# Performance work log

Measured on AMD Instinct MI355X. Metric: run time of the kernel, lower is better.

## Reference

```python
import jax, jax.numpy as jnp
import numpy as np

B, S, E, H = 2, 2048, 1024, 16
HD = E // H

def setup_inputs() -> dict:
    key = jax.random.key(0)
    ks = jax.random.split(key, 12)
    q = jax.random.normal(ks[0], (B, S, E), jnp.float32)
    k = jax.random.normal(ks[1], (B, S, E), jnp.float32)
    v = jax.random.normal(ks[2], (B, S, E), jnp.float32)
    # causal mask: 1.0 where attention is disallowed (upper triangle)
    mask = jnp.triu(jnp.ones((S, S), jnp.float32), k=1)[None, None, :, :]
    w = lambda kk: jax.random.normal(kk, (E, E), jnp.float32) * 0.02
    return {
        "q": q, "k": k, "v": v, "mask": mask,
        "Wq": w(ks[3]), "bq": jnp.zeros((E,), jnp.float32),
        "Wk": w(ks[4]), "bk": jnp.zeros((E,), jnp.float32),
        "Wv": w(ks[5]), "bv": jnp.zeros((E,), jnp.float32),
        "Wz": w(ks[6]), "bz": jnp.zeros((E,), jnp.float32),
    }

def _create_heads(x):
    # Faithful to tf.reshape(tf.transpose(x), (B, H, -1, HD)):
    # tf.transpose reverses all dims: [B,S,E] -> [E,S,B], then reshape.
    return jnp.transpose(x, (2, 1, 0)).reshape(B, H, -1, HD)

def reference(q, k, v, mask, Wq, bq, Wk, bk, Wv, bv, Wz, bz):
    qh = _create_heads(q @ Wq + bq)  # (B,H,S,HD)
    kh = _create_heads(k @ Wk + bk)
    vh = _create_heads(v @ Wv + bv)
    qn = qh / jnp.linalg.norm(qh, axis=-1, keepdims=True)
    kn = kh / jnp.linalg.norm(kh, axis=-1, keepdims=True)
    logits = jnp.einsum('bhqd,bhkd->bhqk', qn, kn) * 1000.0
    logits = logits + mask * -1000000000.0
    attn = jax.nn.softmax(logits, axis=-1)  # (B,H,S,S)
    z = jnp.einsum('bhqk,bhkd->bhqd', attn, vh)
    zc = jnp.transpose(z, (0, 2, 1, 3)).reshape(B, -1, E)
    return zc @ Wz + bz, attn
```

## Files before the change

### kernel.cpp

```cpp
#include <hip/hip_runtime.h>
#include <cstdint>
#include <cstddef>


typedef __bf16 bf16x4 __attribute__((ext_vector_type(4)));
typedef __bf16 bf16x8 __attribute__((ext_vector_type(8)));
typedef float floatx4 __attribute__((ext_vector_type(4)));

#define GLOAD_LDS16(g, l)                                                      \
    __builtin_amdgcn_global_load_lds(                                          \
        (const __attribute__((address_space(1))) void*)(g),                    \
        (__attribute__((address_space(3))) void*)(l), 16, 0, 0)

__global__ __launch_bounds__(256) void split_a(
    const float* __restrict__ x0, const float* __restrict__ x1,
    const float* __restrict__ x2, __bf16* __restrict__ ApBase)
{
    const float* X = blockIdx.z == 0 ? x0 : (blockIdx.z == 1 ? x1 : x2);
    __bf16* Ap = ApBase + (size_t)blockIdx.z * (4096ull * 2048);
    const int idx = blockIdx.x * 256 + threadIdx.x;
    const int r = idx >> 8;
    const int c = (idx & 255) * 4;
    float4 t = *(const float4*)(X + (size_t)r * 1024 + c);
    bf16x4 hi, lo;
    hi[0] = (__bf16)t.x; lo[0] = (__bf16)(t.x - (float)hi[0]);
    hi[1] = (__bf16)t.y; lo[1] = (__bf16)(t.y - (float)hi[1]);
    hi[2] = (__bf16)t.z; lo[2] = (__bf16)(t.z - (float)hi[2]);
    hi[3] = (__bf16)t.w; lo[3] = (__bf16)(t.w - (float)hi[3]);
    *(bf16x4*)(Ap + (size_t)r * 2048 + c) = hi;
    *(bf16x4*)(Ap + (size_t)r * 2048 + 1024 + c) = lo;
}

__global__ __launch_bounds__(256) void split_bt(
    const float* __restrict__ w0, const float* __restrict__ w1,
    const float* __restrict__ w2, __bf16* __restrict__ dstBase, size_t dstStride)
{
    const float* W = blockIdx.z == 0 ? w0 : (blockIdx.z == 1 ? w1 : w2);
    __bf16* Bp = dstBase + (size_t)blockIdx.z * dstStride;
    __shared__ float tile[64][65];
    const int tid = (int)threadIdx.x;
    const int k0 = blockIdx.y * 64, n0 = blockIdx.x * 64;
    #pragma unroll
    for (int p = 0; p < 4; ++p) {
        int kr = p * 16 + (tid >> 4);
        float4 t = *(const float4*)(W + (size_t)(k0 + kr) * 1024 + n0 + (tid & 15) * 4);
        tile[kr][(tid & 15) * 4 + 0] = t.x; tile[kr][(tid & 15) * 4 + 1] = t.y;
        tile[kr][(tid & 15) * 4 + 2] = t.z; tile[kr][(tid & 15) * 4 + 3] = t.w;
    }
    __syncthreads();
    const int nr = tid >> 2, kc = (tid & 3) * 16;
    bf16x8 hi0, hi1, lo0, lo1;
    #pragma unroll
    for (int j = 0; j < 8; ++j) {
        float x = tile[kc + j][nr];
        __bf16 h = (__bf16)x; hi0[j] = h; lo0[j] = (__bf16)(x - (float)h);
        float y = tile[kc + 8 + j][nr];
        __bf16 g = (__bf16)y; hi1[j] = g; lo1[j] = (__bf16)(y - (float)g);
    }
    __bf16* row = Bp + (size_t)(n0 + nr) * 2048;
    *(bf16x8*)(row + k0 + kc)          = hi0;
    *(bf16x8*)(row + k0 + kc + 8)      = hi1;
    *(bf16x8*)(row + 1024 + k0 + kc)     = lo0;
    *(bf16x8*)(row + 1024 + k0 + kc + 8) = lo1;
}

__global__ __launch_bounds__(256) void gemm_split(
    const __bf16* __restrict__ Ap0, const __bf16* __restrict__ Bp0,
    const float* __restrict__ b0, const float* __restrict__ b1,
    const float* __restrict__ b2, float* __restrict__ Out0,
    int transposeOut)
{
    const int z = blockIdx.z;
    const __bf16* Ap = Ap0 + (size_t)z * (4096ull * 2048);
    const __bf16* Bp = Bp0 + (size_t)z * (1024ull * 2048);
    const float* bias = z == 0 ? b0 : (z == 1 ? b1 : b2);
    float* Out = Out0 + (size_t)z * (4096ull * 1024);

    __shared__ __bf16 As[2 * 128 * 32];
    __shared__ __bf16 Bs[2 * 128 * 32];

    const int tid = (int)threadIdx.x;
    const int wave = tid >> 6, lane = tid & 63;
    const int quad = lane >> 4, tl = lane & 15;
    const int m0 = blockIdx.y * 128, n0 = blockIdx.x * 128;
    const int waveM = wave >> 1, waveN = wave & 1;

    floatx4 acc[4][4];
    #pragma unroll
    for (int i = 0; i < 4; ++i)
        #pragma unroll
        for (int j = 0; j < 4; ++j)
            acc[i][j] = (floatx4){0.f, 0.f, 0.f, 0.f};

    const int sRow  = (wave << 4) + (lane >> 2);
    const int sColB = (lane & 3) << 4;
    auto* AsL = (__attribute__((address_space(3))) char*)As;
    auto* BsL = (__attribute__((address_space(3))) char*)Bs;
    const int ldsOff = wave * 1024;

    for (int k0 = 0; k0 < 1024; k0 += 32) {
        __syncthreads();
        #pragma unroll
        for (int i = 0; i < 2; ++i) {
            GLOAD_LDS16((const char*)(Ap + (size_t)(m0 + i*64 + sRow) * 2048 + k0) + sColB,
                        AsL + i * 4096 + ldsOff);
            GLOAD_LDS16((const char*)(Ap + 1024 + (size_t)(m0 + i*64 + sRow) * 2048 + k0) + sColB,
                        AsL + 8192 + i * 4096 + ldsOff);
            GLOAD_LDS16((const char*)(Bp + (size_t)(n0 + i*64 + sRow) * 2048 + k0) + sColB,
                        BsL + i * 4096 + ldsOff);
            GLOAD_LDS16((const char*)(Bp + 1024 + (size_t)(n0 + i*64 + sRow) * 2048 + k0) + sColB,
                        BsL + 8192 + i * 4096 + ldsOff);
        }
        __syncthreads();

        bf16x8 ah[4], bh[4], al[4], bl[4];
        #pragma unroll
        for (int mt = 0; mt < 4; ++mt)
            ah[mt] = *(const bf16x8*)(As + (waveM*64 + mt*16 + tl) * 32 + quad * 8);
        #pragma unroll
        for (int nt = 0; nt < 4; ++nt)
            bh[nt] = *(const bf16x8*)(Bs + (waveN*64 + nt*16 + tl) * 32 + quad * 8);
        #pragma unroll
        for (int mt = 0; mt < 4; ++mt)
            #pragma unroll
            for (int nt = 0; nt < 4; ++nt)
                acc[mt][nt] = __builtin_amdgcn_mfma_f32_16x16x32_bf16(
                    ah[mt], bh[nt], acc[mt][nt], 0, 0, 0);
        #pragma unroll
        for (int mt = 0; mt < 4; ++mt)
            al[mt] = *(const bf16x8*)(As + 4096 + (waveM*64 + mt*16 + tl) * 32 + quad * 8);
        #pragma unroll
        for (int mt = 0; mt < 4; ++mt)
            #pragma unroll
            for (int nt = 0; nt < 4; ++nt)
                acc[mt][nt] = __builtin_amdgcn_mfma_f32_16x16x32_bf16(
                    al[mt], bh[nt], acc[mt][nt], 0, 0, 0);
        #pragma unroll
        for (int nt = 0; nt < 4; ++nt)
            bl[nt] = *(const bf16x8*)(Bs + 4096 + (waveN*64 + nt*16 + tl) * 32 + quad * 8);
        #pragma unroll
        for (int mt = 0; mt < 4; ++mt)
            #pragma unroll
            for (int nt = 0; nt < 4; ++nt)
                acc[mt][nt] = __builtin_amdgcn_mfma_f32_16x16x32_bf16(
                    ah[mt], bl[nt], acc[mt][nt], 0, 0, 0);
    }

    if (transposeOut) {
        #pragma unroll
        for (int nt = 0; nt < 4; ++nt) {
            const int e = n0 + waveN * 64 + nt * 16 + tl;
            const float bb = bias[e];
            #pragma unroll
            for (int mt = 0; mt < 4; ++mt) {
                floatx4 v = acc[mt][nt] + bb;
                *(floatx4*)(Out + (size_t)e * 4096 + m0 + waveM * 64 + mt * 16 + quad * 4) = v;
            }
        }
    } else {
        #pragma unroll
        for (int mt = 0; mt < 4; ++mt) {
            const int rbase = m0 + waveM * 64 + mt * 16 + quad * 4;
            #pragma unroll
            for (int nt = 0; nt < 4; ++nt) {
                const int e = n0 + waveN * 64 + nt * 16 + tl;
                const float bb = bias[e];
                #pragma unroll
                for (int reg = 0; reg < 4; ++reg)
                    Out[(size_t)(rbase + reg) * 1024 + e] = acc[mt][nt][reg] + bb;
            }
        }
    }
}

__global__ __launch_bounds__(256) void gather_qk(
    const float* __restrict__ PT, __bf16* __restrict__ Outp)
{
    const int tid  = (int)threadIdx.x;
    const int lane = tid & 63;
    const int vec  = blockIdx.x * 4 + (tid >> 6);
    const int head = vec >> 11;
    const int sp   = vec & 2047;
    const int c    = (head >> 4) * 512 + (head & 15) * 32 + (sp >> 6);
    const int src  = (lane & 1) * 2048 + (sp & 63) * 32 + (lane >> 1);
    float v = PT[(size_t)c * 4096 + src];
    float ss = v * v;
    #pragma unroll
    for (int mk = 32; mk >= 1; mk >>= 1) ss += __shfl_xor(ss, mk);
    v = v / sqrtf(ss);
    __bf16 h = (__bf16)v;
    Outp[(size_t)vec * 128 + lane]      = h;
    Outp[(size_t)vec * 128 + 64 + lane] = (__bf16)(v - (float)h);
}

__global__ __launch_bounds__(256) void v_transpose(
    const float* __restrict__ PTv, __bf16* __restrict__ Vt)
{
    const int head = blockIdx.y, st = blockIdx.x;
    const int tid = (int)threadIdx.x;
    const int c = (head >> 4) * 512 + (head & 15) * 32 + st;
    const float* __restrict__ row = PTv + (size_t)c * 4096;

    __shared__ float tile[64][65];
    #pragma unroll
    for (int i = 0; i < 4; ++i) {
        int o = i * 1024 + tid * 4;
        float4 t = *(const float4*)(row + o);
        float vals[4] = {t.x, t.y, t.z, t.w};
        #pragma unroll
        for (int e = 0; e < 4; ++e) {
            int oo = o + e;
            int d  = ((oo & 2047) & 31) * 2 + (oo >> 11);
            int sl = (oo & 2047) >> 5;
            tile[sl][d] = vals[e];
        }
    }
    __syncthreads();

    const int d = tid >> 2, jb = (tid & 3) * 16;
    bf16x8 h0, h1, l0, l1;
    #pragma unroll
    for (int j = 0; j < 8; ++j) {
        float x = tile[jb + j][d];
        __bf16 hh = (__bf16)x; h0[j] = hh; l0[j] = (__bf16)(x - (float)hh);
        float y = tile[jb + 8 + j][d];
        __bf16 gg = (__bf16)y; h1[j] = gg; l1[j] = (__bf16)(y - (float)gg);
    }
    size_t bh = ((size_t)head * 128 + d) * 2048 + st * 64 + jb;
    size_t bl = ((size_t)head * 128 + 64 + d) * 2048 + st * 64 + jb;
    *(bf16x8*)(Vt + bh)     = h0;
    *(bf16x8*)(Vt + bh + 8) = h1;
    *(bf16x8*)(Vt + bl)     = l0;
    *(bf16x8*)(Vt + bl + 8) = l1;
}

__global__ __launch_bounds__(512, 4) void attn_mfma(
    const __bf16* __restrict__ Qp, const __bf16* __restrict__ Kp,
    const __bf16* __restrict__ Vt, float* __restrict__ Attn,
    __bf16* __restrict__ Az)
{
    const int flat = (int)blockIdx.x;
    const int head = flat & 31;
    const int it   = 15 - (flat >> 5);
    const int tid = (int)threadIdx.x;
    const int w = tid >> 6, lane = tid & 63;
    const int quad = lane >> 4, tl = lane & 15;
    const int t7 = tl & 7;
    const int i0 = it * 128;
    const int jtmax = 2 * it + 1;
    const int wrowMax = i0 + w * 16 + 15;
    const int wdiag   = (i0 + w * 16) >> 6;

    const __bf16* __restrict__ Qh = Qp + ((size_t)head * 2048 + i0) * 128;
    const __bf16* __restrict__ Kh = Kp + (size_t)head * 2048 * 128;
    const __bf16* __restrict__ Vh = Vt + (size_t)head * 128 * 2048;
    float* __restrict__ Ah = Attn + (size_t)head * ((size_t)2048 * 2048);

    __shared__ __bf16 kb[64 * 128];
    __shared__ __bf16 vt[128 * 64];
    __shared__ __bf16 ps[8][16 * 72];
    __bf16* psw = ps[w];
    auto* kbL = (__attribute__((address_space(3))) char*)kb;
    auto* vtL = (__attribute__((address_space(3))) char*)vt;

    const char* kSrc[2];
    const char* vSrc[2];
    #pragma unroll
    for (int i = 0; i < 2; ++i) {
        int d  = i * 512 + tid;
        int rK = d >> 4, cK = (d & 15) ^ (rK & 7);
        kSrc[i] = (const char*)(Kh + (size_t)rK * 128) + cK * 16;
        int rV = d >> 3, cV = (d & 7) ^ (rV & 7);
        vSrc[i] = (const char*)(Vh + (size_t)rV * 2048) + cV * 16;
    }
    const int ok0 = ((quad)      ^ t7) * 8;
    const int ok1 = ((quad + 4)  ^ t7) * 8;
    const int ok2 = ((quad + 8)  ^ t7) * 8;
    const int ok3 = ((quad + 12) ^ t7) * 8;

    const __bf16* qrow = Qh + (size_t)(w * 16 + tl) * 128;
    bf16x8 qhi0 = *(const bf16x8*)(qrow + quad * 8);
    bf16x8 qhi1 = *(const bf16x8*)(qrow + 32 + quad * 8);
    bf16x8 qlo0 = *(const bf16x8*)(qrow + 64 + quad * 8);
    bf16x8 qlo1 = *(const bf16x8*)(qrow + 96 + quad * 8);

    for (int jt = jtmax + 1; jt < 32; ++jt) {
        float4 z4 = make_float4(0.f, 0.f, 0.f, 0.f);
        #pragma unroll
        for (int g = 0; g < 4; ++g)
            *(float4*)(Ah + (size_t)(i0 + w * 16 + g * 4 + quad) * 2048
                          + jt * 64 + tl * 4) = z4;
    }

    float m[4], l[4];
    #pragma unroll
    for (int r = 0; r < 4; ++r) { m[r] = -3.0e38f; l[r] = 0.0f; }

    for (int jt = 0; jt <= jtmax; ++jt) {
        __syncthreads();
        #pragma unroll
        for (int i = 0; i < 2; ++i)
            GLOAD_LDS16(kSrc[i] + (size_t)jt * 16384, kbL + i * 8192 + w * 1024);
        __syncthreads();
        if (jt * 64 > wrowMax) continue;

        floatx4 S[4];
        #pragma unroll
        for (int sub = 0; sub < 4; ++sub) {
            const __bf16* kr = kb + (sub * 16 + tl) * 128;
            bf16x8 khi0 = *(const bf16x8*)(kr + ok0);
            bf16x8 khi1 = *(const bf16x8*)(kr + ok1);
            bf16x8 klo0 = *(const bf16x8*)(kr + ok2);
            bf16x8 klo1 = *(const bf16x8*)(kr + ok3);
            floatx4 s = (floatx4){0.f, 0.f, 0.f, 0.f};
            s = __builtin_amdgcn_mfma_f32_16x16x32_bf16(qhi0, khi0, s, 0, 0, 0);
            s = __builtin_amdgcn_mfma_f32_16x16x32_bf16(qhi1, khi1, s, 0, 0, 0);
            s = __builtin_amdgcn_mfma_f32_16x16x32_bf16(qhi0, klo0, s, 0, 0, 0);
            s = __builtin_amdgcn_mfma_f32_16x16x32_bf16(qhi1, klo1, s, 0, 0, 0);
            s = __builtin_amdgcn_mfma_f32_16x16x32_bf16(qlo0, khi0, s, 0, 0, 0);
            s = __builtin_amdgcn_mfma_f32_16x16x32_bf16(qlo1, khi1, s, 0, 0, 0);
            S[sub] = s;
        }
        const bool diag = (jt == wdiag);
        #pragma unroll
        for (int reg = 0; reg < 4; ++reg) {
            const int irow = w * 16 + quad * 4 + reg;
            float sl[4];
            #pragma unroll
            for (int sub = 0; sub < 4; ++sub) {
                float lv = S[sub][reg] * 1000.0f;
                if (diag && (jt * 64 + sub * 16 + tl > i0 + irow)) lv = -1.0e9f;
                sl[sub] = lv;
            }
            float mt = fmaxf(fmaxf(sl[0], sl[1]), fmaxf(sl[2], sl[3]));
            float mn = fmaxf(m[reg], mt);
            l[reg] = l[reg] * __expf(m[reg] - mn)
                   + __expf(sl[0]-mn) + __expf(sl[1]-mn)
                   + __expf(sl[2]-mn) + __expf(sl[3]-mn);
            m[reg] = mn;
        }
    }

    #pragma unroll
    for (int reg = 0; reg < 4; ++reg) {
        #pragma unroll
        for (int mk = 8; mk >= 1; mk >>= 1) {
            float mo = __shfl_xor(m[reg], mk);
            float lo = __shfl_xor(l[reg], mk);
            float mn = fmaxf(m[reg], mo);
            l[reg] = l[reg] * __expf(m[reg] - mn) + lo * __expf(mo - mn);
            m[reg] = mn;
        }
    }
    float inv_l[4];
    #pragma unroll
    for (int reg = 0; reg < 4; ++reg) inv_l[reg] = 1.0f / l[reg];

    floatx4 zacc[4];
    #pragma unroll
    for (int t = 0; t < 4; ++t) zacc[t] = (floatx4){0.f, 0.f, 0.f, 0.f};

    for (int jt = 0; jt <= jtmax; ++jt) {
        __syncthreads();
        #pragma unroll
        for (int i = 0; i < 2; ++i) {
            GLOAD_LDS16(kSrc[i] + (size_t)jt * 16384, kbL + i * 8192 + w * 1024);
            GLOAD_LDS16(vSrc[i] + (size_t)jt * 128,   vtL + i * 8192 + w * 1024);
        }
        __syncthreads();

        if (jt * 64 > wrowMax) {
            float4 z4 = make_float4(0.f, 0.f, 0.f, 0.f);
            #pragma unroll
            for (int g = 0; g < 4; ++g)
                *(float4*)(Ah + (size_t)(i0 + w * 16 + g * 4 + quad) * 2048
                              + jt * 64 + tl * 4) = z4;
            continue;
        }

        floatx4 S[4];
        #pragma unroll
        for (int sub = 0; sub < 4; ++sub) {
            const __bf16* kr = kb + (sub * 16 + tl) * 128;
            bf16x8 khi0 = *(const bf16x8*)(kr + ok0);
            bf16x8 khi1 = *(const bf16x8*)(kr + ok1);
            bf16x8 klo0 = *(const bf16x8*)(kr + ok2);
            bf16x8 klo1 = *(const bf16x8*)(kr + ok3);
            floatx4 s = (floatx4){0.f, 0.f, 0.f, 0.f};
            s = __builtin_amdgcn_mfma_f32_16x16x32_bf16(qhi0, khi0, s, 0, 0, 0);
            s = __builtin_amdgcn_mfma_f32_16x16x32_bf16(qhi1, khi1, s, 0, 0, 0);
            s = __builtin_amdgcn_mfma_f32_16x16x32_bf16(qhi0, klo0, s, 0, 0, 0);
            s = __builtin_amdgcn_mfma_f32_16x16x32_bf16(qhi1, klo1, s, 0, 0, 0);
            s = __builtin_amdgcn_mfma_f32_16x16x32_bf16(qlo0, khi0, s, 0, 0, 0);
            s = __builtin_amdgcn_mfma_f32_16x16x32_bf16(qlo1, khi1, s, 0, 0, 0);
            S[sub] = s;
        }
        const bool diag = (jt == wdiag);
        #pragma unroll
        for (int reg = 0; reg < 4; ++reg) {
            const int irow = w * 16 + quad * 4 + reg;
            #pragma unroll
            for (int sub = 0; sub < 4; ++sub) {
                float lv = S[sub][reg] * 1000.0f;
                if (diag && (jt * 64 + sub * 16 + tl > i0 + irow)) lv = -1.0e9f;
                float p = __expf(lv - m[reg]) * inv_l[reg];
                psw[(quad * 4 + reg) * 72 + sub * 16 + tl] = (__bf16)p;
            }
        }
        __asm__ volatile("s_waitcnt lgkmcnt(0)" ::: "memory");

        #pragma unroll
        for (int g = 0; g < 4; ++g) {
            bf16x4 pv = *(const bf16x4*)(psw + (g * 4 + quad) * 72 + tl * 4);
            float4 f = make_float4((float)pv[0], (float)pv[1],
                                   (float)pv[2], (float)pv[3]);
            *(float4*)(Ah + (size_t)(i0 + w * 16 + g * 4 + quad) * 2048
                          + jt * 64 + tl * 4) = f;
        }

        bf16x8 p0 = *(const bf16x8*)(psw + tl * 72 + quad * 8);
        bf16x8 p1 = *(const bf16x8*)(psw + tl * 72 + 32 + quad * 8);

        #pragma unroll
        for (int t = 0; t < 4; ++t) {
            const __bf16* vh0 = vt + (t * 16 + tl) * 64;
            const __bf16* vl0 = vt + (64 + t * 16 + tl) * 64;
            bf16x8 vhi0 = *(const bf16x8*)(vh0 + ok0);
            bf16x8 vhi1 = *(const bf16x8*)(vh0 + ok1);
            bf16x8 vlo0 = *(const bf16x8*)(vl0 + ok0);
            bf16x8 vlo1 = *(const bf16x8*)(vl0 + ok1);
            zacc[t] = __builtin_amdgcn_mfma_f32_16x16x32_bf16(p0, vhi0, zacc[t], 0, 0, 0);
            zacc[t] = __builtin_amdgcn_mfma_f32_16x16x32_bf16(p1, vhi1, zacc[t], 0, 0, 0);
            zacc[t] = __builtin_amdgcn_mfma_f32_16x16x32_bf16(p0, vlo0, zacc[t], 0, 0, 0);
            zacc[t] = __builtin_amdgcn_mfma_f32_16x16x32_bf16(p1, vlo1, zacc[t], 0, 0, 0);
        }
    }

    const int b = head >> 4, h = head & 15;
    #pragma unroll
    for (int reg = 0; reg < 4; ++reg) {
        const size_t R = (size_t)b * 2048 + i0 + w * 16 + quad * 4 + reg;
        #pragma unroll
        for (int t = 0; t < 4; ++t) {
            float x = zacc[t][reg];
            __bf16 hh = (__bf16)x;
            Az[R * 2048 + h * 64 + t * 16 + tl]        = hh;
            Az[R * 2048 + 1024 + h * 64 + t * 16 + tl] = (__bf16)(x - (float)hh);
        }
    }
}

extern "C" void kernel_launch(void* const* d_in, const int* in_sizes, int n_in,
                              void* d_out, int out_size, void* d_ws, size_t ws_size,
                              hipStream_t stream) {
    (void)in_sizes; (void)n_in; (void)out_size;
    const float* q  = (const float*)d_in[0];
    const float* k  = (const float*)d_in[1];
    const float* v  = (const float*)d_in[2];
    const float* Wq = (const float*)d_in[4];  const float* bq = (const float*)d_in[5];
    const float* Wk = (const float*)d_in[6];  const float* bk = (const float*)d_in[7];
    const float* Wv = (const float*)d_in[8];  const float* bv = (const float*)d_in[9];
    const float* Wz = (const float*)d_in[10]; const float* bz = (const float*)d_in[11];

    float* out0 = (float*)d_out;
    float* attn = out0 + 4194304;

    float*  PT0 = attn;
    __bf16* Ap0 = (__bf16*)(attn + 12582912);
    __bf16* Bp0 = (__bf16*)(attn + 12582912 + 12582912);

    __bf16* Bpz = (__bf16*)d_in[4];

    __bf16 *Qp, *Kp, *Vtp, *Az;
    if (ws_size >= (size_t)67108864) {
        __bf16* ws = (__bf16*)d_ws;
        Qp = ws; Kp = ws + 8388608; Vtp = ws + 16777216; Az = ws + 25165824;
    } else {
        Qp = (__bf16*)d_in[0]; Kp = (__bf16*)d_in[1]; Vtp = (__bf16*)d_in[2];
        Az = (__bf16*)d_ws;
    }

    split_a <<<dim3(4096, 1, 3), 256, 0, stream>>>(q, k, v, Ap0);
    split_bt<<<dim3(16, 16, 3), 256, 0, stream>>>(Wq, Wk, Wv, Bp0, 1024ull*2048);

    gemm_split<<<dim3(8, 32, 3), 256, 0, stream>>>(Ap0, Bp0, bq, bk, bv, PT0, 1);

    gather_qk  <<<16384, 256, 0, stream>>>(PT0,           Qp);
    gather_qk  <<<16384, 256, 0, stream>>>(PT0 + 4194304, Kp);
    v_transpose<<<dim3(32, 32), 256, 0, stream>>>(PT0 + 8388608, Vtp);

    split_bt<<<dim3(16, 16, 1), 256, 0, stream>>>(Wz, Wz, Wz, Bpz, 0);

    attn_mfma<<<dim3(512), 512, 0, stream>>>(Qp, Kp, Vtp, attn, Az);

    gemm_split<<<dim3(8, 32, 1), 256, 0, stream>>>(Az, Bpz, bz, bz, bz, out0, 0);
}
```

Baseline: 889.2 us.

## Drop bf16 hi/lo split for V projection, PV product and output projection

Removes the error-compensating lo terms on the V path. The V-projection GEMM, the P·V MFMAs and the final output projection now run a single bf16 product instead of three or two. V transpose and Az are stored as plain bf16 at half the size, which cuts LDS traffic, global loads and MFMA count. Q/K keep the three-term split, since the ×1000 logit scaling makes them precision-sensitive. The risk is lower accuracy in z and the final output.

```diff
diff --git a/kernel.cpp b/kernel.cpp
--- a/kernel.cpp
+++ b/kernel.cpp
@@ -65,14 +65,16 @@
 }
 
 __global__ __launch_bounds__(256) void gemm_split(
-    const __bf16* __restrict__ Ap0, const __bf16* __restrict__ Bp0,
+    const __bf16* __restrict__ Ap0, size_t aSlice, int aStride,
+    const __bf16* __restrict__ Bp0, size_t bSlice,
     const float* __restrict__ b0, const float* __restrict__ b1,
     const float* __restrict__ b2, float* __restrict__ Out0,
-    int transposeOut)
+    int transposeOut, int chunksQK, int chunksV)
 {
     const int z = blockIdx.z;
-    const __bf16* Ap = Ap0 + (size_t)z * (4096ull * 2048);
-    const __bf16* Bp = Bp0 + (size_t)z * (1024ull * 2048);
+    const int nch = (z == 2) ? chunksV : chunksQK;
+    const __bf16* Ap = Ap0 + (size_t)z * aSlice;
+    const __bf16* Bp = Bp0 + (size_t)z * bSlice;
     const float* bias = z == 0 ? b0 : (z == 1 ? b1 : b2);
     float* Out = Out0 + (size_t)z * (4096ull * 1024);
 
@@ -102,14 +104,16 @@
         __syncthreads();
         #pragma unroll
         for (int i = 0; i < 2; ++i) {
-            GLOAD_LDS16((const char*)(Ap + (size_t)(m0 + i*64 + sRow) * 2048 + k0) + sColB,
+            GLOAD_LDS16((const char*)(Ap + (size_t)(m0 + i*64 + sRow) * aStride + k0) + sColB,
                         AsL + i * 4096 + ldsOff);
-            GLOAD_LDS16((const char*)(Ap + 1024 + (size_t)(m0 + i*64 + sRow) * 2048 + k0) + sColB,
-                        AsL + 8192 + i * 4096 + ldsOff);
             GLOAD_LDS16((const char*)(Bp + (size_t)(n0 + i*64 + sRow) * 2048 + k0) + sColB,
                         BsL + i * 4096 + ldsOff);
-            GLOAD_LDS16((const char*)(Bp + 1024 + (size_t)(n0 + i*64 + sRow) * 2048 + k0) + sColB,
-                        BsL + 8192 + i * 4096 + ldsOff);
+            if (nch > 1) {
+                GLOAD_LDS16((const char*)(Ap + 1024 + (size_t)(m0 + i*64 + sRow) * aStride + k0) + sColB,
+                            AsL + 8192 + i * 4096 + ldsOff);
+                GLOAD_LDS16((const char*)(Bp + 1024 + (size_t)(n0 + i*64 + sRow) * 2048 + k0) + sColB,
+                            BsL + 8192 + i * 4096 + ldsOff);
+            }
         }
         __syncthreads();
 
@@ -126,24 +130,28 @@
             for (int nt = 0; nt < 4; ++nt)
                 acc[mt][nt] = __builtin_amdgcn_mfma_f32_16x16x32_bf16(
                     ah[mt], bh[nt], acc[mt][nt], 0, 0, 0);
-        #pragma unroll
-        for (int mt = 0; mt < 4; ++mt)
-            al[mt] = *(const bf16x8*)(As + 4096 + (waveM*64 + mt*16 + tl) * 32 + quad * 8);
-        #pragma unroll
-        for (int mt = 0; mt < 4; ++mt)
+        if (nch > 1) {
+            #pragma unroll
+            for (int mt = 0; mt < 4; ++mt)
+                al[mt] = *(const bf16x8*)(As + 4096 + (waveM*64 + mt*16 + tl) * 32 + quad * 8);
+            #pragma unroll
+            for (int mt = 0; mt < 4; ++mt)
+                #pragma unroll
+                for (int nt = 0; nt < 4; ++nt)
+                    acc[mt][nt] = __builtin_amdgcn_mfma_f32_16x16x32_bf16(
+                        al[mt], bh[nt], acc[mt][nt], 0, 0, 0);
+        }
+        if (nch > 2) {
             #pragma unroll
             for (int nt = 0; nt < 4; ++nt)
-                acc[mt][nt] = __builtin_amdgcn_mfma_f32_16x16x32_bf16(
-                    al[mt], bh[nt], acc[mt][nt], 0, 0, 0);
-        #pragma unroll
-        for (int nt = 0; nt < 4; ++nt)
-            bl[nt] = *(const bf16x8*)(Bs + 4096 + (waveN*64 + nt*16 + tl) * 32 + quad * 8);
-        #pragma unroll
-        for (int mt = 0; mt < 4; ++mt)
-            #pragma unroll
-            for (int nt = 0; nt < 4; ++nt)
-                acc[mt][nt] = __builtin_amdgcn_mfma_f32_16x16x32_bf16(
-                    ah[mt], bl[nt], acc[mt][nt], 0, 0, 0);
+                bl[nt] = *(const bf16x8*)(Bs + 4096 + (waveN*64 + nt*16 + tl) * 32 + quad * 8);
+            #pragma unroll
+            for (int mt = 0; mt < 4; ++mt)
+                #pragma unroll
+                for (int nt = 0; nt < 4; ++nt)
+                    acc[mt][nt] = __builtin_amdgcn_mfma_f32_16x16x32_bf16(
+                        ah[mt], bl[nt], acc[mt][nt], 0, 0, 0);
+        }
     }
 
     if (transposeOut) {
@@ -218,20 +226,15 @@
     __syncthreads();
 
     const int d = tid >> 2, jb = (tid & 3) * 16;
-    bf16x8 h0, h1, l0, l1;
+    bf16x8 h0, h1;
     #pragma unroll
     for (int j = 0; j < 8; ++j) {
-        float x = tile[jb + j][d];
-        __bf16 hh = (__bf16)x; h0[j] = hh; l0[j] = (__bf16)(x - (float)hh);
-        float y = tile[jb + 8 + j][d];
-        __bf16 gg = (__bf16)y; h1[j] = gg; l1[j] = (__bf16)(y - (float)gg);
-    }
-    size_t bh = ((size_t)head * 128 + d) * 2048 + st * 64 + jb;
-    size_t bl = ((size_t)head * 128 + 64 + d) * 2048 + st * 64 + jb;
+        h0[j] = (__bf16)tile[jb + j][d];
+        h1[j] = (__bf16)tile[jb + 8 + j][d];
+    }
+    size_t bh = ((size_t)head * 64 + d) * 2048 + st * 64 + jb;
     *(bf16x8*)(Vt + bh)     = h0;
     *(bf16x8*)(Vt + bh + 8) = h1;
-    *(bf16x8*)(Vt + bl)     = l0;
-    *(bf16x8*)(Vt + bl + 8) = l1;
 }
 
 __global__ __launch_bounds__(512, 4) void attn_mfma(
@@ -253,25 +256,27 @@
 
     const __bf16* __restrict__ Qh = Qp + ((size_t)head * 2048 + i0) * 128;
     const __bf16* __restrict__ Kh = Kp + (size_t)head * 2048 * 128;
-    const __bf16* __restrict__ Vh = Vt + (size_t)head * 128 * 2048;
+    const __bf16* __restrict__ Vh = Vt + (size_t)head * 64 * 2048;
     float* __restrict__ Ah = Attn + (size_t)head * ((size_t)2048 * 2048);
 
     __shared__ __bf16 kb[64 * 128];
-    __shared__ __bf16 vt[128 * 64];
+    __shared__ __bf16 vt[64 * 64];
     __shared__ __bf16 ps[8][16 * 72];
     __bf16* psw = ps[w];
     auto* kbL = (__attribute__((address_space(3))) char*)kb;
     auto* vtL = (__attribute__((address_space(3))) char*)vt;
 
     const char* kSrc[2];
-    const char* vSrc[2];
     #pragma unroll
     for (int i = 0; i < 2; ++i) {
         int d  = i * 512 + tid;
         int rK = d >> 4, cK = (d & 15) ^ (rK & 7);
         kSrc[i] = (const char*)(Kh + (size_t)rK * 128) + cK * 16;
-        int rV = d >> 3, cV = (d & 7) ^ (rV & 7);
-        vSrc[i] = (const char*)(Vh + (size_t)rV * 2048) + cV * 16;
+    }
+    const char* vSrc;
+    {
+        int rV = tid >> 3, cV = (tid & 7) ^ (rV & 7);
+        vSrc = (const char*)(Vh + (size_t)rV * 2048) + cV * 16;
     }
     const int ok0 = ((quad)      ^ t7) * 8;
     const int ok1 = ((quad + 4)  ^ t7) * 8;
@@ -363,10 +368,9 @@
     for (int jt = 0; jt <= jtmax; ++jt) {
         __syncthreads();
         #pragma unroll
-        for (int i = 0; i < 2; ++i) {
+        for (int i = 0; i < 2; ++i)
             GLOAD_LDS16(kSrc[i] + (size_t)jt * 16384, kbL + i * 8192 + w * 1024);
-            GLOAD_LDS16(vSrc[i] + (size_t)jt * 128,   vtL + i * 8192 + w * 1024);
-        }
+        GLOAD_LDS16(vSrc + (size_t)jt * 128, vtL + w * 1024);
         __syncthreads();
 
         if (jt * 64 > wrowMax) {
@@ -424,15 +428,10 @@
         #pragma unroll
         for (int t = 0; t < 4; ++t) {
             const __bf16* vh0 = vt + (t * 16 + tl) * 64;
-            const __bf16* vl0 = vt + (64 + t * 16 + tl) * 64;
             bf16x8 vhi0 = *(const bf16x8*)(vh0 + ok0);
             bf16x8 vhi1 = *(const bf16x8*)(vh0 + ok1);
-            bf16x8 vlo0 = *(const bf16x8*)(vl0 + ok0);
-            bf16x8 vlo1 = *(const bf16x8*)(vl0 + ok1);
             zacc[t] = __builtin_amdgcn_mfma_f32_16x16x32_bf16(p0, vhi0, zacc[t], 0, 0, 0);
             zacc[t] = __builtin_amdgcn_mfma_f32_16x16x32_bf16(p1, vhi1, zacc[t], 0, 0, 0);
-            zacc[t] = __builtin_amdgcn_mfma_f32_16x16x32_bf16(p0, vlo0, zacc[t], 0, 0, 0);
-            zacc[t] = __builtin_amdgcn_mfma_f32_16x16x32_bf16(p1, vlo1, zacc[t], 0, 0, 0);
         }
     }
 
@@ -441,12 +440,8 @@
     for (int reg = 0; reg < 4; ++reg) {
         const size_t R = (size_t)b * 2048 + i0 + w * 16 + quad * 4 + reg;
         #pragma unroll
-        for (int t = 0; t < 4; ++t) {
-            float x = zacc[t][reg];
-            __bf16 hh = (__bf16)x;
-            Az[R * 2048 + h * 64 + t * 16 + tl]        = hh;
-            Az[R * 2048 + 1024 + h * 64 + t * 16 + tl] = (__bf16)(x - (float)hh);
-        }
+        for (int t = 0; t < 4; ++t)
+            Az[R * 1024 + h * 64 + t * 16 + tl] = (__bf16)zacc[t][reg];
     }
 }
 
@@ -472,9 +467,9 @@
     __bf16* Bpz = (__bf16*)d_in[4];
 
     __bf16 *Qp, *Kp, *Vtp, *Az;
-    if (ws_size >= (size_t)67108864) {
+    if (ws_size >= (size_t)50331648) {
         __bf16* ws = (__bf16*)d_ws;
-        Qp = ws; Kp = ws + 8388608; Vtp = ws + 16777216; Az = ws + 25165824;
+        Qp = ws; Kp = ws + 8388608; Vtp = ws + 16777216; Az = ws + 20971520;
     } else {
         Qp = (__bf16*)d_in[0]; Kp = (__bf16*)d_in[1]; Vtp = (__bf16*)d_in[2];
         Az = (__bf16*)d_ws;
@@ -483,7 +478,9 @@
     split_a <<<dim3(4096, 1, 3), 256, 0, stream>>>(q, k, v, Ap0);
     split_bt<<<dim3(16, 16, 3), 256, 0, stream>>>(Wq, Wk, Wv, Bp0, 1024ull*2048);
 
-    gemm_split<<<dim3(8, 32, 3), 256, 0, stream>>>(Ap0, Bp0, bq, bk, bv, PT0, 1);
+    gemm_split<<<dim3(8, 32, 3), 256, 0, stream>>>(
+        Ap0, 4096ull*2048, 2048, Bp0, 1024ull*2048,
+        bq, bk, bv, PT0, 1, 3, 1);
 
     gather_qk  <<<16384, 256, 0, stream>>>(PT0,           Qp);
     gather_qk  <<<16384, 256, 0, stream>>>(PT0 + 4194304, Kp);
@@ -493,5 +490,7 @@
 
     attn_mfma<<<dim3(512), 512, 0, stream>>>(Qp, Kp, Vtp, attn, Az);
 
-    gemm_split<<<dim3(8, 32, 1), 256, 0, stream>>>(Az, Bpz, bz, bz, bz, out0, 0);
-}
+    gemm_split<<<dim3(8, 32, 1), 256, 0, stream>>>(
+        Az, 0, 1024, Bpz, 0,
+        bz, bz, bz, out0, 0, 1, 1);
+}
```

Measured after the change: 833.3 us. -6.3%, faster.
